# Performance work log

Measured on AMD Instinct MI355X. Metric: run time of the kernel, lower is better.

Reference implementation:

```python
import jax, jax.numpy as jnp
import numpy as np

N_DOCS = 1_000_000
N_FEAT = 136
BATCH = 1_000_000

# MSLR feature column indices used by the original module
COL_DOCLEN = 14      # metadata docLength
COL_WHOLE_LEN = 16   # used for avgDocLength statistic
COL_TF = 24          # term frequency feature
COL_INLINK = 127
COL_OUTLINK = 128
COL_PAGERANK = 129


def setup_inputs() -> dict:
    key = jax.random.key(0)
    k_feat, k_idx, kb, kpr, kin, kout = jax.random.split(key, 6)
    global_features = jax.random.uniform(k_feat, (N_DOCS, N_FEAT), dtype=jnp.float32)
    batch_indices = jax.random.randint(k_idx, (BATCH,), 0, N_DOCS)
    return {
        "batch_indices": batch_indices,
        "global_features": global_features,
        "k1": jnp.asarray(3.5, jnp.float32),
        "b": jnp.asarray(0.5, jnp.float32),
        "bm25_weight": jnp.asarray(1.0, jnp.float32),
        "page_rank": jnp.asarray(0.2, jnp.float32),
        "in_link": jnp.asarray(0.1, jnp.float32),
        "out_link": jnp.asarray(0.1, jnp.float32),
        "freshness": jnp.asarray(1.0, jnp.float32),
    }


def reference(batch_indices, global_features, k1, b, bm25_weight, page_rank,
              in_link, out_link, freshness):
    # Global doc statistics (computed once, like fetch_total_doc_statistics_mslr)
    avg_doc_len = jnp.mean(global_features[:, COL_WHOLE_LEN])
    total_docs = jnp.float32(global_features.shape[0])

    # Vectorized gather of per-doc features for the batch
    rows = global_features[batch_indices]            # [B, F]
    term_freq = rows[:, COL_TF]                      # [B]
    doc_length = rows[:, COL_DOCLEN]                 # [B]
    pr = rows[:, COL_PAGERANK]
    inl = rows[:, COL_INLINK]
    outl = rows[:, COL_OUTLINK]

    # In the original, num_docs_with_term == total corpus size (constant)
    num_docs_with_term = total_docs
    idf_term = jnp.log((total_docs - num_docs_with_term + 0.5) / (num_docs_with_term + 0.5) + 1.0)

    numerator = term_freq * (k1 + 1.0)
    denominator = term_freq + k1 * (1.0 - b + b * (doc_length / avg_doc_len))
    bm25_score = idf_term * (numerator / denominator)

    pagerank_score = page_rank * pr + in_link * inl + out_link * outl

    # torch.rand(1).item() per doc -> a random constant per doc, scaled by freshness
    fresh_noise = jax.random.uniform(jax.random.key(1), (batch_indices.shape[0],), dtype=jnp.float32)
    freshness_score = fresh_noise * freshness

    scores = bm25_weight * bm25_score + pagerank_score + freshness_score
    return scores[:, None]  # [B, 1]
```

## Files before the change

### kernel.cpp

```cpp
#include <hip/hip_runtime.h>
#include <stdint.h>

#define N_FEAT 136
#define COL_DOCLEN 14
#define COL_WHOLE_LEN 16
#define COL_TF 24
#define COL_INLINK 127
#define COL_OUTLINK 128
#define COL_PAGERANK 129

__device__ __forceinline__ void threefry2x32(uint32_t k0, uint32_t k1,
                                             uint32_t& x0, uint32_t& x1) {
  const uint32_t ks0 = k0, ks1 = k1, ks2 = k0 ^ k1 ^ 0x1BD11BDAu;
  x0 += ks0; x1 += ks1;
#define TF_ROUND(r) { x0 += x1; x1 = (x1 << (r)) | (x1 >> (32 - (r))); x1 ^= x0; }
  TF_ROUND(13) TF_ROUND(15) TF_ROUND(26) TF_ROUND(6)
  x0 += ks1; x1 += ks2 + 1u;
  TF_ROUND(17) TF_ROUND(29) TF_ROUND(16) TF_ROUND(24)
  x0 += ks2; x1 += ks0 + 2u;
  TF_ROUND(13) TF_ROUND(15) TF_ROUND(26) TF_ROUND(6)
  x0 += ks0; x1 += ks1 + 3u;
  TF_ROUND(17) TF_ROUND(29) TF_ROUND(16) TF_ROUND(24)
  x0 += ks1; x1 += ks2 + 4u;
  TF_ROUND(13) TF_ROUND(15) TF_ROUND(26) TF_ROUND(6)
  x0 += ks2; x1 += ks0 + 5u;
#undef TF_ROUND
}

__device__ __forceinline__ float tf_noise(uint32_t i) {
  uint32_t x0 = 0u, x1 = i;
  threefry2x32(0u, 1u, x0, x1);
  const uint32_t bits = x0 ^ x1;
  return __uint_as_float((bits >> 9) | 0x3f800000u) - 1.0f;
}

__global__ void doc_pass_kernel(const float* __restrict__ gf,
                                const float* __restrict__ p_prw,
                                const float* __restrict__ p_inw,
                                const float* __restrict__ p_outw,
                                float* __restrict__ tf_a,
                                float* __restrict__ dl_a,
                                float* __restrict__ link_a,
                                float* __restrict__ sum,
                                int n_docs) {
  const int j = blockIdx.x * blockDim.x + threadIdx.x;
  float wl = 0.f;
  if (j < n_docs) {
    const size_t base = (size_t)j * N_FEAT;
    const float dl  = gf[base + COL_DOCLEN];
    wl              = gf[base + COL_WHOLE_LEN];
    const float tf  = gf[base + COL_TF];
    const float inl = gf[base + COL_INLINK];
    const float2 op = *reinterpret_cast<const float2*>(gf + base + COL_OUTLINK);
    tf_a[j]   = tf;
    dl_a[j]   = dl;
    link_a[j] = p_prw[0] * op.y + p_inw[0] * inl + p_outw[0] * op.x;
  }
  for (int off = 32; off > 0; off >>= 1) wl += __shfl_down(wl, off, 64);
  __shared__ float ws_[4];
  const int lane = threadIdx.x & 63, wave = threadIdx.x >> 6;
  if (lane == 0) ws_[wave] = wl;
  __syncthreads();
  if (threadIdx.x == 0) atomicAdd(sum, ws_[0] + ws_[1] + ws_[2] + ws_[3]);
}

__global__ void doc_score_kernel(const float* __restrict__ tf_a,
                                 const float* __restrict__ dl_a,
                                 const float* __restrict__ link_a,
                                 const float* __restrict__ p_k1,
                                 const float* __restrict__ p_b,
                                 const float* __restrict__ p_bm25w,
                                 const float* __restrict__ col_sum,
                                 float* __restrict__ s_doc,
                                 int n_docs, float total_docs) {
  const int j = blockIdx.x * blockDim.x + threadIdx.x;
  if (j >= n_docs) return;
  const float k1 = p_k1[0];
  const float b  = p_b[0];
  const float bm25w = p_bm25w[0];
  const float avg_doc_len = col_sum[0] / total_docs;
  const float idf = logf(0.5f / (total_docs + 0.5f) + 1.0f);
  const float tf = tf_a[j];
  const float dl = dl_a[j];
  const float numer = tf * (k1 + 1.0f);
  const float denom = tf + k1 * (1.0f - b + b * (dl / avg_doc_len));
  const float bm25 = idf * (numer / denom);
  s_doc[j] = bm25w * bm25 + link_a[j];
}

__global__ void gather_kernel(const int* __restrict__ idx,
                              const float* __restrict__ s_doc,
                              const float* __restrict__ p_fresh,
                              float* __restrict__ out, int batch) {
  const int t = blockIdx.x * blockDim.x + threadIdx.x;
  int i = t * 4;
  const float fresh = p_fresh[0];
  if (i + 3 < batch) {
    const int4 id = *reinterpret_cast<const int4*>(idx + i);
    float4 r;
    r.x = s_doc[id.x] + tf_noise((uint32_t)(i + 0)) * fresh;
    r.y = s_doc[id.y] + tf_noise((uint32_t)(i + 1)) * fresh;
    r.z = s_doc[id.z] + tf_noise((uint32_t)(i + 2)) * fresh;
    r.w = s_doc[id.w] + tf_noise((uint32_t)(i + 3)) * fresh;
    *reinterpret_cast<float4*>(out + i) = r;
  } else {
    for (; i < batch; ++i)
      out[i] = s_doc[idx[i]] + tf_noise((uint32_t)i) * fresh;
  }
}

__global__ void col16_sum_kernel(const float* __restrict__ gf, float* __restrict__ sum,
                                 int n_docs) {
  int stride = gridDim.x * blockDim.x;
  float v = 0.f;
  for (int j = blockIdx.x * blockDim.x + threadIdx.x; j < n_docs; j += stride)
    v += gf[(size_t)j * N_FEAT + COL_WHOLE_LEN];
  for (int off = 32; off > 0; off >>= 1) v += __shfl_down(v, off, 64);
  __shared__ float ws[4];
  int lane = threadIdx.x & 63, wave = threadIdx.x >> 6;
  if (lane == 0) ws[wave] = v;
  __syncthreads();
  if (threadIdx.x == 0) {
    float t = 0.f;
    int nw = blockDim.x >> 6;
    for (int w = 0; w < nw; ++w) t += ws[w];
    atomicAdd(sum, t);
  }
}

__global__ void score_kernel(const int* __restrict__ idx,
                             const float* __restrict__ gf,
                             const float* __restrict__ p_k1,
                             const float* __restrict__ p_b,
                             const float* __restrict__ p_bm25w,
                             const float* __restrict__ p_prw,
                             const float* __restrict__ p_inw,
                             const float* __restrict__ p_outw,
                             const float* __restrict__ p_fresh,
                             const float* __restrict__ col_sum,
                             float* __restrict__ out,
                             int batch, float total_docs) {
  int i = blockIdx.x * blockDim.x + threadIdx.x;
  if (i >= batch) return;
  const float k1 = p_k1[0];
  const float b  = p_b[0];
  const float bm25w = p_bm25w[0];
  const float avg_doc_len = col_sum[0] / total_docs;
  const float idf = logf(0.5f / (total_docs + 0.5f) + 1.0f);
  const size_t base = (size_t)idx[i] * N_FEAT;
  const float tf   = gf[base + COL_TF];
  const float dl   = gf[base + COL_DOCLEN];
  const float pr   = gf[base + COL_PAGERANK];
  const float inl  = gf[base + COL_INLINK];
  const float outl = gf[base + COL_OUTLINK];
  const float numer = tf * (k1 + 1.0f);
  const float denom = tf + k1 * (1.0f - b + b * (dl / avg_doc_len));
  const float bm25 = idf * (numer / denom);
  out[i] = bm25w * bm25 + p_prw[0] * pr + p_inw[0] * inl + p_outw[0] * outl
         + tf_noise((uint32_t)i) * p_fresh[0];
}

extern "C" void kernel_launch(void* const* d_in, const int* in_sizes, int n_in,
                              void* d_out, int out_size, void* d_ws, size_t ws_size,
                              hipStream_t stream) {
  const int*   batch_indices = (const int*)d_in[0];
  const float* gf            = (const float*)d_in[1];
  const float* k1    = (const float*)d_in[2];
  const float* b     = (const float*)d_in[3];
  const float* bm25w = (const float*)d_in[4];
  const float* prw   = (const float*)d_in[5];
  const float* inw   = (const float*)d_in[6];
  const float* outw  = (const float*)d_in[7];
  const float* fresh = (const float*)d_in[8];
  float* out = (float*)d_out;

  const int batch  = in_sizes[0];
  const int n_docs = in_sizes[1] / N_FEAT;

  float* ws      = (float*)d_ws;
  float* col_sum = ws;
  float* tf_a    = ws + 64;
  float* dl_a    = tf_a + n_docs;
  float* link_a  = dl_a + n_docs;
  float* s_doc   = link_a + n_docs;
  const size_t need = (64 + 4 * (size_t)n_docs) * sizeof(float);

  hipMemsetAsync(col_sum, 0, sizeof(float), stream);

  const int tpb = 256;
  if (ws_size >= need) {
    const int b_doc = (n_docs + tpb - 1) / tpb;
    doc_pass_kernel<<<b_doc, tpb, 0, stream>>>(gf, prw, inw, outw,
                                               tf_a, dl_a, link_a, col_sum, n_docs);
    doc_score_kernel<<<b_doc, tpb, 0, stream>>>(tf_a, dl_a, link_a, k1, b, bm25w,
                                                col_sum, s_doc, n_docs, (float)n_docs);
    const int b_gat = ((batch + 3) / 4 + tpb - 1) / tpb;
    gather_kernel<<<b_gat, tpb, 0, stream>>>(batch_indices, s_doc, fresh, out, batch);
  } else {
    col16_sum_kernel<<<1024, tpb, 0, stream>>>(gf, col_sum, n_docs);
    const int blocks = (batch + tpb - 1) / tpb;
    score_kernel<<<blocks, tpb, 0, stream>>>(
        batch_indices, gf, k1, b, bm25w, prw, inw, outw, fresh,
        col_sum, out, batch, (float)n_docs);
  }
}
```

Baseline: 674.3 us.

## Stage full document rows into LDS via global_load_lds in doc pass

The doc pass kernel now loads 112 contiguous rows per block into shared memory with direct global-to-LDS 16-byte loads, then extracts the needed columns from LDS, using two threads per row. This replaces scattered strided per-thread column loads with fully coalesced streaming. It reads the entire row, including unused columns, and the large LDS footprint limits occupancy.

```diff
diff --git a/kernel.cpp b/kernel.cpp
--- a/kernel.cpp
+++ b/kernel.cpp
@@ -8,6 +8,12 @@
 #define COL_INLINK 127
 #define COL_OUTLINK 128
 #define COL_PAGERANK 129
+
+#define ROWS_PER_BLOCK 112
+#define TPB 256
+
+typedef const __attribute__((address_space(1))) void* gas_ptr;
+typedef __attribute__((address_space(3))) void* las_ptr;
 
 __device__ __forceinline__ void threefry2x32(uint32_t k0, uint32_t k1,
                                              uint32_t& x0, uint32_t& x1) {
@@ -34,34 +40,58 @@
   return __uint_as_float((bits >> 9) | 0x3f800000u) - 1.0f;
 }
 
-__global__ void doc_pass_kernel(const float* __restrict__ gf,
-                                const float* __restrict__ p_prw,
-                                const float* __restrict__ p_inw,
-                                const float* __restrict__ p_outw,
-                                float* __restrict__ tf_a,
-                                float* __restrict__ dl_a,
-                                float* __restrict__ link_a,
-                                float* __restrict__ sum,
-                                int n_docs) {
-  const int j = blockIdx.x * blockDim.x + threadIdx.x;
+__global__ __launch_bounds__(TPB) void doc_pass_kernel(
+    const float* __restrict__ gf,
+    const float* __restrict__ p_prw,
+    const float* __restrict__ p_inw,
+    const float* __restrict__ p_outw,
+    float* __restrict__ tf_a,
+    float* __restrict__ dl_a,
+    float* __restrict__ link_a,
+    float* __restrict__ sum,
+    int n_docs) {
+  __shared__ float lds[ROWS_PER_BLOCK * N_FEAT];
+  const int r0 = blockIdx.x * ROWS_PER_BLOCK;
+  int rows = n_docs - r0;
+  if (rows > ROWS_PER_BLOCK) rows = ROWS_PER_BLOCK;
+  const int n4 = rows * (N_FEAT / 4);
+  const float* gbase = gf + (size_t)r0 * N_FEAT;
+
+  for (int i = threadIdx.x; i < n4; i += TPB) {
+    __builtin_amdgcn_global_load_lds((gas_ptr)(gbase + 4 * (size_t)i),
+                                     (las_ptr)(lds + 4 * i), 16, 0, 0);
+  }
+  __syncthreads();
+
+  const int t = threadIdx.x;
+  const int r = t >> 1;
   float wl = 0.f;
-  if (j < n_docs) {
-    const size_t base = (size_t)j * N_FEAT;
-    const float dl  = gf[base + COL_DOCLEN];
-    wl              = gf[base + COL_WHOLE_LEN];
-    const float tf  = gf[base + COL_TF];
-    const float inl = gf[base + COL_INLINK];
-    const float2 op = *reinterpret_cast<const float2*>(gf + base + COL_OUTLINK);
-    tf_a[j]   = tf;
-    dl_a[j]   = dl;
-    link_a[j] = p_prw[0] * op.y + p_inw[0] * inl + p_outw[0] * op.x;
-  }
+  if (r < rows) {
+    const float* row = &lds[r * N_FEAT];
+    if ((t & 1) == 0) {
+      const float dl = row[COL_DOCLEN];
+      wl             = row[COL_WHOLE_LEN];
+      const float tf = row[COL_TF];
+      tf_a[r0 + r] = tf;
+      dl_a[r0 + r] = dl;
+    } else {
+      const float inl  = row[COL_INLINK];
+      const float outl = row[COL_OUTLINK];
+      const float pr   = row[COL_PAGERANK];
+      link_a[r0 + r] = p_prw[0] * pr + p_inw[0] * inl + p_outw[0] * outl;
+    }
+  }
+
   for (int off = 32; off > 0; off >>= 1) wl += __shfl_down(wl, off, 64);
-  __shared__ float ws_[4];
-  const int lane = threadIdx.x & 63, wave = threadIdx.x >> 6;
+  __shared__ float ws_[TPB / 64];
+  const int lane = t & 63, wave = t >> 6;
   if (lane == 0) ws_[wave] = wl;
   __syncthreads();
-  if (threadIdx.x == 0) atomicAdd(sum, ws_[0] + ws_[1] + ws_[2] + ws_[3]);
+  if (t == 0) {
+    float tot = 0.f;
+    for (int w = 0; w < TPB / 64; ++w) tot += ws_[w];
+    atomicAdd(sum, tot);
+  }
 }
 
 __global__ void doc_score_kernel(const float* __restrict__ tf_a,
@@ -187,19 +217,19 @@
 
   hipMemsetAsync(col_sum, 0, sizeof(float), stream);
 
-  const int tpb = 256;
   if (ws_size >= need) {
-    const int b_doc = (n_docs + tpb - 1) / tpb;
-    doc_pass_kernel<<<b_doc, tpb, 0, stream>>>(gf, prw, inw, outw,
+    const int b_doc = (n_docs + ROWS_PER_BLOCK - 1) / ROWS_PER_BLOCK;
+    doc_pass_kernel<<<b_doc, TPB, 0, stream>>>(gf, prw, inw, outw,
                                                tf_a, dl_a, link_a, col_sum, n_docs);
-    doc_score_kernel<<<b_doc, tpb, 0, stream>>>(tf_a, dl_a, link_a, k1, b, bm25w,
-                                                col_sum, s_doc, n_docs, (float)n_docs);
-    const int b_gat = ((batch + 3) / 4 + tpb - 1) / tpb;
-    gather_kernel<<<b_gat, tpb, 0, stream>>>(batch_indices, s_doc, fresh, out, batch);
+    const int b_sc = (n_docs + TPB - 1) / TPB;
+    doc_score_kernel<<<b_sc, TPB, 0, stream>>>(tf_a, dl_a, link_a, k1, b, bm25w,
+                                               col_sum, s_doc, n_docs, (float)n_docs);
+    const int b_gat = ((batch + 3) / 4 + TPB - 1) / TPB;
+    gather_kernel<<<b_gat, TPB, 0, stream>>>(batch_indices, s_doc, fresh, out, batch);
   } else {
-    col16_sum_kernel<<<1024, tpb, 0, stream>>>(gf, col_sum, n_docs);
-    const int blocks = (batch + tpb - 1) / tpb;
-    score_kernel<<<blocks, tpb, 0, stream>>>(
+    col16_sum_kernel<<<1024, TPB, 0, stream>>>(gf, col_sum, n_docs);
+    const int blocks = (batch + TPB - 1) / TPB;
+    score_kernel<<<blocks, TPB, 0, stream>>>(
         batch_indices, gf, k1, b, bm25w, prw, inw, outw, fresh,
         col_sum, out, batch, (float)n_docs);
   }
```

New measurement: 730.2 us. 1.08x slower.

## Stream whole feature matrix with coalesced float4 grid-stride scan

Applied to the files above, without the earlier changes.

Replaces the per-document strided column reads with a grid-stride loop over the entire feature matrix as float4 elements. Each thread finds its row and column chunk and writes the needed columns to compact arrays, while the link-score combination moves into the doc-score kernel. The aim is fully coalesced streaming reads instead of scattered 4-byte loads that each touch a separate cache line. In exchange, every byte of the 544MB matrix is read rather than only the lines holding the wanted columns, there are integer divisions per element, and the workspace needs an extra array.

```diff
diff --git a/kernel.cpp b/kernel.cpp
--- a/kernel.cpp
+++ b/kernel.cpp
@@ -2,12 +2,16 @@
 #include <stdint.h>
 
 #define N_FEAT 136
+#define F4_PER_ROW 34
 #define COL_DOCLEN 14
 #define COL_WHOLE_LEN 16
 #define COL_TF 24
 #define COL_INLINK 127
 #define COL_OUTLINK 128
 #define COL_PAGERANK 129
+
+#define TPB 256
+#define SCAN_BLOCKS 2048
 
 __device__ __forceinline__ void threefry2x32(uint32_t k0, uint32_t k1,
                                              uint32_t& x0, uint32_t& x1) {
@@ -34,42 +38,48 @@
   return __uint_as_float((bits >> 9) | 0x3f800000u) - 1.0f;
 }
 
-__global__ void doc_pass_kernel(const float* __restrict__ gf,
-                                const float* __restrict__ p_prw,
-                                const float* __restrict__ p_inw,
-                                const float* __restrict__ p_outw,
-                                float* __restrict__ tf_a,
-                                float* __restrict__ dl_a,
-                                float* __restrict__ link_a,
-                                float* __restrict__ sum,
-                                int n_docs) {
-  const int j = blockIdx.x * blockDim.x + threadIdx.x;
+__global__ __launch_bounds__(TPB) void scan_kernel(
+    const float4* __restrict__ gf4,
+    float* __restrict__ tf_a,
+    float* __restrict__ dl_a,
+    float* __restrict__ inl_a,
+    float2* __restrict__ op_a,
+    float* __restrict__ sum,
+    int n4) {
+  const int nthreads = gridDim.x * blockDim.x;
   float wl = 0.f;
-  if (j < n_docs) {
-    const size_t base = (size_t)j * N_FEAT;
-    const float dl  = gf[base + COL_DOCLEN];
-    wl              = gf[base + COL_WHOLE_LEN];
-    const float tf  = gf[base + COL_TF];
-    const float inl = gf[base + COL_INLINK];
-    const float2 op = *reinterpret_cast<const float2*>(gf + base + COL_OUTLINK);
-    tf_a[j]   = tf;
-    dl_a[j]   = dl;
-    link_a[j] = p_prw[0] * op.y + p_inw[0] * inl + p_outw[0] * op.x;
+  for (int g = blockIdx.x * blockDim.x + threadIdx.x; g < n4; g += nthreads) {
+    const float4 v = gf4[g];
+    const int r = g / F4_PER_ROW;
+    const int c = g - r * F4_PER_ROW;
+    if (c == 4)       wl += v.x;
+    else if (c == 3)  dl_a[r] = v.z;
+    else if (c == 6)  tf_a[r] = v.x;
+    else if (c == 31) inl_a[r] = v.w;
+    else if (c == 32) op_a[r] = make_float2(v.x, v.y);
   }
   for (int off = 32; off > 0; off >>= 1) wl += __shfl_down(wl, off, 64);
-  __shared__ float ws_[4];
+  __shared__ float ws_[TPB / 64];
   const int lane = threadIdx.x & 63, wave = threadIdx.x >> 6;
   if (lane == 0) ws_[wave] = wl;
   __syncthreads();
-  if (threadIdx.x == 0) atomicAdd(sum, ws_[0] + ws_[1] + ws_[2] + ws_[3]);
+  if (threadIdx.x == 0) {
+    float tot = 0.f;
+    for (int w = 0; w < TPB / 64; ++w) tot += ws_[w];
+    atomicAdd(sum, tot);
+  }
 }
 
 __global__ void doc_score_kernel(const float* __restrict__ tf_a,
                                  const float* __restrict__ dl_a,
-                                 const float* __restrict__ link_a,
+                                 const float* __restrict__ inl_a,
+                                 const float2* __restrict__ op_a,
                                  const float* __restrict__ p_k1,
                                  const float* __restrict__ p_b,
                                  const float* __restrict__ p_bm25w,
+                                 const float* __restrict__ p_prw,
+                                 const float* __restrict__ p_inw,
+                                 const float* __restrict__ p_outw,
                                  const float* __restrict__ col_sum,
                                  float* __restrict__ s_doc,
                                  int n_docs, float total_docs) {
@@ -82,10 +92,11 @@
   const float idf = logf(0.5f / (total_docs + 0.5f) + 1.0f);
   const float tf = tf_a[j];
   const float dl = dl_a[j];
+  const float2 op = op_a[j];
   const float numer = tf * (k1 + 1.0f);
   const float denom = tf + k1 * (1.0f - b + b * (dl / avg_doc_len));
   const float bm25 = idf * (numer / denom);
-  s_doc[j] = bm25w * bm25 + link_a[j];
+  s_doc[j] = bm25w * bm25 + p_prw[0] * op.y + p_inw[0] * inl_a[j] + p_outw[0] * op.x;
 }
 
 __global__ void gather_kernel(const int* __restrict__ idx,
@@ -181,25 +192,27 @@
   float* col_sum = ws;
   float* tf_a    = ws + 64;
   float* dl_a    = tf_a + n_docs;
-  float* link_a  = dl_a + n_docs;
-  float* s_doc   = link_a + n_docs;
-  const size_t need = (64 + 4 * (size_t)n_docs) * sizeof(float);
+  float* inl_a   = dl_a + n_docs;
+  float2* op_a   = (float2*)(inl_a + n_docs);
+  float* s_doc   = (float*)(op_a + n_docs);
+  const size_t need = (64 + 6 * (size_t)n_docs) * sizeof(float);
 
   hipMemsetAsync(col_sum, 0, sizeof(float), stream);
 
-  const int tpb = 256;
-  if (ws_size >= need) {
-    const int b_doc = (n_docs + tpb - 1) / tpb;
-    doc_pass_kernel<<<b_doc, tpb, 0, stream>>>(gf, prw, inw, outw,
-                                               tf_a, dl_a, link_a, col_sum, n_docs);
-    doc_score_kernel<<<b_doc, tpb, 0, stream>>>(tf_a, dl_a, link_a, k1, b, bm25w,
-                                                col_sum, s_doc, n_docs, (float)n_docs);
-    const int b_gat = ((batch + 3) / 4 + tpb - 1) / tpb;
-    gather_kernel<<<b_gat, tpb, 0, stream>>>(batch_indices, s_doc, fresh, out, batch);
+  if (ws_size >= need && (n_docs & 1) == 0) {
+    const int n4 = n_docs * F4_PER_ROW;
+    scan_kernel<<<SCAN_BLOCKS, TPB, 0, stream>>>(
+        (const float4*)gf, tf_a, dl_a, inl_a, op_a, col_sum, n4);
+    const int b_sc = (n_docs + TPB - 1) / TPB;
+    doc_score_kernel<<<b_sc, TPB, 0, stream>>>(tf_a, dl_a, inl_a, op_a,
+                                               k1, b, bm25w, prw, inw, outw,
+                                               col_sum, s_doc, n_docs, (float)n_docs);
+    const int b_gat = ((batch + 3) / 4 + TPB - 1) / TPB;
+    gather_kernel<<<b_gat, TPB, 0, stream>>>(batch_indices, s_doc, fresh, out, batch);
   } else {
-    col16_sum_kernel<<<1024, tpb, 0, stream>>>(gf, col_sum, n_docs);
-    const int blocks = (batch + tpb - 1) / tpb;
-    score_kernel<<<blocks, tpb, 0, stream>>>(
+    col16_sum_kernel<<<1024, TPB, 0, stream>>>(gf, col_sum, n_docs);
+    const int blocks = (batch + TPB - 1) / TPB;
+    score_kernel<<<blocks, TPB, 0, stream>>>(
         batch_indices, gf, k1, b, bm25w, prw, inw, outw, fresh,
         col_sum, out, batch, (float)n_docs);
   }
```

After: 756.3 us. 12.2% more time.
